# Performance work log

Hardware: AMD Instinct MI355X
Metric: run time of the kernel (lower is better)

## Reference

```python
import jax, jax.numpy as jnp
import numpy as np

D_MODEL = 1024
N, L = 4, 2048


def setup_inputs() -> dict:
    key = jax.random.key(0)
    ks = jax.random.split(key, 8)
    s = 0.1
    return {
        "X": jax.random.normal(ks[0], (N, L, D_MODEL), dtype=jnp.float32),
        "W_Q1": jax.random.normal(ks[1], (D_MODEL, D_MODEL), dtype=jnp.float32) * s,
        "W_K1": jax.random.normal(ks[2], (D_MODEL, D_MODEL), dtype=jnp.float32) * s,
        "W_V1": jax.random.normal(ks[3], (D_MODEL, D_MODEL), dtype=jnp.float32) * s,
        "W_Q2": jax.random.normal(ks[4], (D_MODEL, D_MODEL), dtype=jnp.float32) * s,
        "W_K2": jax.random.normal(ks[5], (D_MODEL, D_MODEL), dtype=jnp.float32) * s,
        "W_V2": jax.random.normal(ks[6], (D_MODEL, D_MODEL), dtype=jnp.float32) * s,
        "W_O": jax.random.normal(ks[7], (D_MODEL, 1), dtype=jnp.float32) * s,
        "b_O": jnp.zeros((1, 1), dtype=jnp.float32),
    }


def _attn_block(H, W_Q, W_K, W_V):
    # H: (N, L, D); single-head scaled dot-product attention
    Q = jnp.einsum('nld,dk->nlk', H, W_Q)
    K = jnp.einsum('nld,dk->nlk', H, W_K)
    V = jnp.einsum('nld,dk->nlk', H, W_V)
    scale = jnp.sqrt(jnp.asarray(Q.shape[-1], Q.dtype))
    scores = jnp.einsum('nqd,nkd->nqk', Q, K) / scale  # (N, L, L)
    attn = jax.nn.softmax(scores, axis=-1)
    return jnp.einsum('nqk,nkd->nqd', attn, V)


def reference(X, W_Q1, W_K1, W_V1, W_Q2, W_K2, W_V2, W_O, b_O):
    H1 = _attn_block(X, W_Q1, W_K1, W_V1)
    H2 = _attn_block(H1, W_Q2, W_K2, W_V2)
    pooled = jnp.mean(H2, axis=1)            # (N, D)
    logits = pooled @ W_O + b_O              # (N, 1)
    return jax.nn.sigmoid(logits).squeeze(-1)  # (N,)
```

## Files before the change

### kernel.cpp

```cpp
#include <hip/hip_runtime.h>
#include <hip/hip_bf16.h>
#include <cstdint>


#define DEVFN __device__ __forceinline__

typedef __attribute__((ext_vector_type(8))) short bf16x8;
typedef __attribute__((ext_vector_type(8))) _Float16 f16x8;
typedef __attribute__((ext_vector_type(4))) float f32x4;
typedef unsigned short u16;

DEVFN u16 f2bf(float f) {
    uint32_t x = __float_as_uint(f);
    x += 0x7fffu + ((x >> 16) & 1u);
    return (u16)(x >> 16);
}
DEVFN float bf2f(u16 u) { return __uint_as_float(((uint32_t)u) << 16); }

DEVFN void gload_lds16(const void* g, void* l) {
    __builtin_amdgcn_global_load_lds(
        (const __attribute__((address_space(1))) void*)g,
        (__attribute__((address_space(3))) void*)l, 16, 0, 0);
}

#define MFMA16 __builtin_amdgcn_mfma_f32_16x16x32_bf16

template<int EPI, bool TBUF>
__global__ __launch_bounds__(256, TBUF ? 3 : 4) void gemmk(
    const u16* __restrict__ A, long long aStride,
    const u16* __restrict__ B, long long bStride,
    void* __restrict__ out0, void* __restrict__ out1,
    const float* __restrict__ zrow, long long cStride,
    int M, int N, int K, int lda, int ldb, int ldc, float scale)
{
    constexpr int ASEC  = 128 * 32;
    constexpr int BUFSZ = ASEC + 128 * 32;
    constexpr int NU    = 4;
    constexpr int NB    = TBUF ? 3 : 2;

    __shared__ __align__(16) u16 L[NB * BUFSZ];
    const int tid  = threadIdx.x;
    const int wave = tid >> 6, lane = tid & 63;

    const int gx = gridDim.x, gy = gridDim.y;
    const int nwg = gx * gy * gridDim.z;
    int flat = (blockIdx.z * gy + blockIdx.y) * gx + blockIdx.x;
    flat = (flat & 7) * (nwg >> 3) + (flat >> 3);
    const int bx = flat % gx, by = (flat / gx) % gy, bz = flat / (gx * gy);

    const u16* pA = A + (size_t)bz * aStride;
    const u16* pB = B + (size_t)bz * bStride;
    const int m0 = by * 128, n0 = bx * 128;

    const u16* src[NU];
    int dst[NU];
#pragma unroll
    for (int q = 0; q < 2; q++) {
        const int s = q * 256 + tid, row = s >> 2, c = (s & 3) ^ ((row >> 1) & 3);
        src[q]     = pA + (size_t)(m0 + row) * lda + c * 8;
        dst[q]     = q * 2048 + wave * 512;
        src[2 + q] = pB + (size_t)(n0 + row) * ldb + c * 8;
        dst[2 + q] = ASEC + q * 2048 + wave * 512;
    }

    const int fr = lane & 15, ch = lane >> 4;
    const int wr = (wave >> 1) * 64, wc = (wave & 1) * 64;

    const int NT = K >> 5;
    f32x4 acc[4][4] = {};

    if constexpr (TBUF) {
#pragma unroll
        for (int u = 0; u < NU; u++) { gload_lds16(src[u], &L[dst[u]]); src[u] += 32; }
#pragma unroll
        for (int u = 0; u < NU; u++) { gload_lds16(src[u], &L[BUFSZ + dst[u]]); src[u] += 32; }
        asm volatile("s_waitcnt vmcnt(4)" ::: "memory");
        __builtin_amdgcn_s_barrier();
        __builtin_amdgcn_sched_barrier(0);

        int cIdx = 0, sIdx = 2;
        for (int kt = 0; kt < NT; ++kt) {
            const int cOff = cIdx * BUFSZ;
            if (kt + 2 < NT) {
                const int sOff = sIdx * BUFSZ;
#pragma unroll
                for (int u = 0; u < NU; u++) { gload_lds16(src[u], &L[sOff + dst[u]]); src[u] += 32; }
            }

            bf16x8 ah[4], bh[4];
#pragma unroll
            for (int i = 0; i < 4; i++) {
                const int r = wr + i * 16 + fr;
                ah[i] = *(const bf16x8*)&L[cOff + r * 32 + ((ch ^ ((r >> 1) & 3)) << 3)];
            }
#pragma unroll
            for (int j = 0; j < 4; j++) {
                const int r = wc + j * 16 + fr;
                bh[j] = *(const bf16x8*)&L[cOff + ASEC + r * 32 + ((ch ^ ((r >> 1) & 3)) << 3)];
            }

#pragma unroll
            for (int i = 0; i < 4; i++)
#pragma unroll
                for (int j = 0; j < 4; j++)
                    acc[i][j] = MFMA16(ah[i], bh[j], acc[i][j], 0, 0, 0);

            if (kt + 1 < NT) {
                if (kt + 2 < NT) asm volatile("s_waitcnt vmcnt(4)" ::: "memory");
                else             asm volatile("s_waitcnt vmcnt(0)" ::: "memory");
                __builtin_amdgcn_s_barrier();
                __builtin_amdgcn_sched_barrier(0);
            }
            cIdx = (cIdx == 2) ? 0 : cIdx + 1;
            sIdx = (sIdx == 2) ? 0 : sIdx + 1;
        }
    } else {
#pragma unroll
        for (int u = 0; u < NU; u++) { gload_lds16(src[u], &L[dst[u]]); src[u] += 32; }
        __syncthreads();

        int cur = 0;
        for (int kt = 0; kt < NT; ++kt) {
            const int cOff = cur * BUFSZ;
            const int sOff = BUFSZ - cOff;
            if (kt + 1 < NT) {
#pragma unroll
                for (int u = 0; u < NU; u++) { gload_lds16(src[u], &L[sOff + dst[u]]); src[u] += 32; }
            }

            bf16x8 ah[4], bh[4];
#pragma unroll
            for (int i = 0; i < 4; i++) {
                const int r = wr + i * 16 + fr;
                ah[i] = *(const bf16x8*)&L[cOff + r * 32 + ((ch ^ ((r >> 1) & 3)) << 3)];
            }
#pragma unroll
            for (int j = 0; j < 4; j++) {
                const int r = wc + j * 16 + fr;
                bh[j] = *(const bf16x8*)&L[cOff + ASEC + r * 32 + ((ch ^ ((r >> 1) & 3)) << 3)];
            }

#pragma unroll
            for (int i = 0; i < 4; i++)
#pragma unroll
                for (int j = 0; j < 4; j++)
                    acc[i][j] = MFMA16(ah[i], bh[j], acc[i][j], 0, 0, 0);

            __syncthreads();
            cur ^= 1;
        }
    }

    if constexpr (EPI == 5) {
#pragma unroll
        for (int i = 0; i < 4; i++)
#pragma unroll
            for (int r = 0; r < 4; r++) {
                const int rowb = m0 + wr + i * 16 + ch * 4 + r;
                float s = 0.f;
#pragma unroll
                for (int j = 0; j < 4; j++) {
                    const int col = n0 + wc + j * 16 + fr;
                    const float e = __expf(acc[i][j][r] * scale - 60.f);
                    s += e;
                    ((u16*)out0)[(size_t)bz * cStride + (size_t)rowb * ldc + col] = f2bf(e);
                }
                s += __shfl_xor(s, 1, 16);
                s += __shfl_xor(s, 2, 16);
                s += __shfl_xor(s, 4, 16);
                s += __shfl_xor(s, 8, 16);
                if (fr == 0)
                    ((float*)out1)[((size_t)bz * 2048 + rowb) * 32 + ((n0 + wc) >> 6)] = s;
            }
    } else if constexpr (EPI == 6) {
#pragma unroll
        for (int i = 0; i < 4; i++)
#pragma unroll
            for (int r = 0; r < 4; r++) {
                const int row = m0 + wr + i * 16 + ch * 4 + r;
                const size_t grow = (size_t)bz * 2048 + row;
                float zp = zrow[grow * 32 + 2 * fr] + zrow[grow * 32 + 2 * fr + 1];
                zp += __shfl_xor(zp, 1, 16);
                zp += __shfl_xor(zp, 2, 16);
                zp += __shfl_xor(zp, 4, 16);
                zp += __shfl_xor(zp, 8, 16);
                const float zi = 1.f / zp;
#pragma unroll
                for (int j = 0; j < 4; j++) {
                    const int col = n0 + wc + j * 16 + fr;
                    ((u16*)out0)[(size_t)bz * cStride + (size_t)row * ldc + col] =
                        f2bf(acc[i][j][r] * zi);
                }
            }
    } else {
#pragma unroll
        for (int i = 0; i < 4; i++)
#pragma unroll
            for (int j = 0; j < 4; j++)
#pragma unroll
                for (int r = 0; r < 4; r++) {
                    const int row = m0 + wr + i * 16 + (lane >> 4) * 4 + r;
                    const int col = n0 + wc + j * 16 + (lane & 15);
                    const float v = acc[i][j][r] * scale;
                    if constexpr (EPI == 3) {
                        ((u16*)out0)[(size_t)bz * cStride + (size_t)row * ldc + col] = f2bf(v);
                    } else {
                        ((_Float16*)out0)[(size_t)bz * cStride + (size_t)row * ldc + col] =
                            (_Float16)v;
                    }
                }
    }
}

__global__ __launch_bounds__(256, 3) void gemm_tv(
    const u16* __restrict__ Xb, const u16* __restrict__ Mt1,
    const u16* __restrict__ Wv1T, u16* __restrict__ Tb, u16* __restrict__ Vtb)
{
    constexpr int ASEC  = 128 * 32;
    constexpr int BUFSZ = ASEC + 128 * 32;
    constexpr int NU    = 4;

    __shared__ __align__(16) u16 L[3 * BUFSZ];
    const int tid  = threadIdx.x;
    const int wave = tid >> 6, lane = tid & 63;

    int flat = blockIdx.x;
    flat = (flat & 7) * 128 + (flat >> 3);
    const int op = flat & 1, t = flat >> 1;
    const u16* pA;
    const u16* pB;
    u16* outp;
    int m0, n0, ldc;
    if (op == 0) {
        pA = Xb;  pB = Mt1;  outp = Tb;  ldc = 1024;
        m0 = (t >> 3) * 128; n0 = (t & 7) * 128;
    } else {
        pA = Wv1T; pB = Xb;  outp = Vtb; ldc = 8192;
        m0 = (t >> 6) * 128; n0 = (t & 63) * 128;
    }

    const u16* src[NU];
    int dst[NU];
#pragma unroll
    for (int q = 0; q < 2; q++) {
        const int s = q * 256 + tid, row = s >> 2, c = (s & 3) ^ ((row >> 1) & 3);
        src[q]     = pA + (size_t)(m0 + row) * 1024 + c * 8;
        dst[q]     = q * 2048 + wave * 512;
        src[2 + q] = pB + (size_t)(n0 + row) * 1024 + c * 8;
        dst[2 + q] = ASEC + q * 2048 + wave * 512;
    }

    const int fr = lane & 15, ch = lane >> 4;
    const int wr = (wave >> 1) * 64, wc = (wave & 1) * 64;

#pragma unroll
    for (int u = 0; u < NU; u++) { gload_lds16(src[u], &L[dst[u]]); src[u] += 32; }
#pragma unroll
    for (int u = 0; u < NU; u++) { gload_lds16(src[u], &L[BUFSZ + dst[u]]); src[u] += 32; }
    asm volatile("s_waitcnt vmcnt(4)" ::: "memory");
    __builtin_amdgcn_s_barrier();
    __builtin_amdgcn_sched_barrier(0);

    f32x4 acc[4][4] = {};
    int cIdx = 0, sIdx = 2;

    for (int kt = 0; kt < 32; ++kt) {
        const int cOff = cIdx * BUFSZ;
        if (kt + 2 < 32) {
            const int sOff = sIdx * BUFSZ;
#pragma unroll
            for (int u = 0; u < NU; u++) { gload_lds16(src[u], &L[sOff + dst[u]]); src[u] += 32; }
        }

        bf16x8 ah[4], bh[4];
#pragma unroll
        for (int i = 0; i < 4; i++) {
            const int r = wr + i * 16 + fr;
            ah[i] = *(const bf16x8*)&L[cOff + r * 32 + ((ch ^ ((r >> 1) & 3)) << 3)];
        }
#pragma unroll
        for (int j = 0; j < 4; j++) {
            const int r = wc + j * 16 + fr;
            bh[j] = *(const bf16x8*)&L[cOff + ASEC + r * 32 + ((ch ^ ((r >> 1) & 3)) << 3)];
        }

#pragma unroll
        for (int i = 0; i < 4; i++)
#pragma unroll
            for (int j = 0; j < 4; j++)
                acc[i][j] = MFMA16(ah[i], bh[j], acc[i][j], 0, 0, 0);

        if (kt + 1 < 32) {
            if (kt + 2 < 32) asm volatile("s_waitcnt vmcnt(4)" ::: "memory");
            else             asm volatile("s_waitcnt vmcnt(0)" ::: "memory");
            __builtin_amdgcn_s_barrier();
            __builtin_amdgcn_sched_barrier(0);
        }
        cIdx = (cIdx == 2) ? 0 : cIdx + 1;
        sIdx = (sIdx == 2) ? 0 : sIdx + 1;
    }

#pragma unroll
    for (int i = 0; i < 4; i++)
#pragma unroll
        for (int j = 0; j < 4; j++)
#pragma unroll
            for (int r = 0; r < 4; r++) {
                const int row = m0 + wr + i * 16 + (lane >> 4) * 4 + r;
                const int col = n0 + wc + j * 16 + (lane & 15);
                outp[(size_t)row * ldc + col] = f2bf(acc[i][j][r]);
            }
}

__global__ __launch_bounds__(256) void prep_all(
    const float* __restrict__ X,
    const float* __restrict__ W0, const float* __restrict__ W1,
    const float* __restrict__ W2, const float* __restrict__ W3,
    const float* __restrict__ Wv1, const float* __restrict__ Wv2,
    const float* __restrict__ wO,
    u16* __restrict__ Xb, u16* __restrict__ Wcat,
    u16* __restrict__ Wv1T, float* __restrict__ wv)
{
    const int blk = blockIdx.x, tid = threadIdx.x;
    __shared__ float t[64][65];

    if (blk < 8192) {
        const size_t i = ((size_t)blk * 256 + tid) * 4;
        const float4 v = *(const float4*)&X[i];
        ushort4 h;
        h.x = f2bf(v.x); h.y = f2bf(v.y); h.z = f2bf(v.z); h.w = f2bf(v.w);
        *(ushort4*)&Xb[i] = h;
    } else if (blk < 12288) {
        const int w = (blk - 8192) >> 10, ib = (blk - 8192) & 1023;
        const float* W = (w == 0) ? W0 : (w == 1) ? W1 : (w == 2) ? W2 : W3;
        u16* o = Wcat + (size_t)w * 1048576;
        const size_t i = ((size_t)ib * 256 + tid) * 4;
        const float4 v = *(const float4*)&W[i];
        ushort4 h;
        h.x = f2bf(v.x); h.y = f2bf(v.y); h.z = f2bf(v.z); h.w = f2bf(v.w);
        *(ushort4*)&o[i] = h;
    } else if (blk < 12544) {
        const int tb = blk - 12288;
        const int r0 = (tb >> 4) * 64, c0 = (tb & 15) * 64;
#pragma unroll
        for (int it = 0; it < 16; it++) {
            const int idx = it * 256 + tid, rr = idx >> 6, cc = idx & 63;
            t[rr][cc] = Wv1[(size_t)(r0 + rr) * 1024 + (c0 + cc)];
        }
        __syncthreads();
#pragma unroll
        for (int it = 0; it < 16; it++) {
            const int idx = it * 256 + tid, nn = idx >> 6, kk = idx & 63;
            Wv1T[(size_t)(c0 + nn) * 1024 + (r0 + kk)] = f2bf(t[kk][nn]);
        }
    } else {
        const int d = (blk - 12544) * 16 + (tid >> 4);
        const int lx = tid & 15;
        const float* row = Wv2 + (size_t)d * 1024;
        float s = 0.f;
#pragma unroll
        for (int it = 0; it < 16; it++) {
            const int j = it * 64 + lx * 4;
            const float4 a = *(const float4*)&row[j];
            const float4 w = *(const float4*)&wO[j];
            s += a.x * w.x + a.y * w.y + a.z * w.z + a.w * w.w;
        }
#pragma unroll
        for (int o = 8; o; o >>= 1) s += __shfl_xor(s, o, 16);
        if (lx == 0) wv[d] = s;
    }
}

__global__ __launch_bounds__(256) void mid_head(
    const _Float16* __restrict__ S, float* __restrict__ part,
    const u16* __restrict__ H1, const float* __restrict__ wv,
    float* __restrict__ u)
{
    const int blk = blockIdx.x, tid = threadIdx.x;
    __shared__ float redm[4], reds[4];

    if (blk < 512) {
        const int b = blk >> 7, chunk = blk & 127;
        const _Float16* Sb = S + (size_t)b * (2048 * 2048) + (size_t)chunk * 16 * 2048;
        float acc[8] = {};

        for (int r = 0; r < 16; r++) {
            const _Float16* row = Sb + (size_t)r * 2048;
            const f16x8 hv = *(const f16x8*)&row[tid * 8];
            float v[8];
#pragma unroll
            for (int j = 0; j < 8; j++) v[j] = (float)hv[j];

            float m = v[0];
#pragma unroll
            for (int j = 1; j < 8; j++) m = fmaxf(m, v[j]);
            for (int o = 32; o; o >>= 1) m = fmaxf(m, __shfl_xor(m, o));
            if ((tid & 63) == 0) redm[tid >> 6] = m;
            __syncthreads();
            m = fmaxf(fmaxf(redm[0], redm[1]), fmaxf(redm[2], redm[3]));

            float e[8], s = 0.f;
#pragma unroll
            for (int j = 0; j < 8; j++) { e[j] = __expf(v[j] - m); s += e[j]; }
            for (int o = 32; o; o >>= 1) s += __shfl_xor(s, o);
            if ((tid & 63) == 0) reds[tid >> 6] = s;
            __syncthreads();
            const float inv = 1.f / (reds[0] + reds[1] + reds[2] + reds[3]);
#pragma unroll
            for (int j = 0; j < 8; j++) acc[j] += e[j] * inv;
            __syncthreads();
        }

        float* p = part + ((size_t)(b * 128 + chunk)) * 2048;
#pragma unroll
        for (int j = 0; j < 8; j++) p[tid * 8 + j] = acc[j];
    } else {
        const int r = (blk - 512) * 16 + (tid >> 4);
        const int lx = tid & 15;
        const u16* row = H1 + (size_t)r * 1024;
        float s = 0.f;
#pragma unroll
        for (int it = 0; it < 8; it++) {
            const int d = it * 128 + lx * 8;
            const bf16x8 h = *(const bf16x8*)&row[d];
#pragma unroll
            for (int j = 0; j < 8; j++) s += bf2f((u16)h[j]) * wv[d + j];
        }
#pragma unroll
        for (int o = 8; o; o >>= 1) s += __shfl_xor(s, o, 16);
        if (lx == 0) u[r] = s;
    }
}

__global__ __launch_bounds__(256) void tail2(
    const float* __restrict__ part, const float* __restrict__ u,
    float* __restrict__ partial)
{
    const int blk = blockIdx.x, tid = threadIdx.x;
    const int b = blk >> 5;
    const int kl = tid & 63;
    const int k = (blk & 31) * 64 + kl;
    const int cg = tid >> 6;
    float s = 0.f;
#pragma unroll 4
    for (int c = 0; c < 32; c++)
        s += part[((size_t)(b * 128 + cg * 32 + c)) * 2048 + k];
    __shared__ float red[4][64];
    red[cg][kl] = s;
    __syncthreads();
    if (cg == 0) {
        float v = (red[0][kl] + red[1][kl] + red[2][kl] + red[3][kl])
                  * u[b * 2048 + k];
        for (int o = 32; o; o >>= 1) v += __shfl_xor(v, o);
        if (kl == 0) partial[blk] = v;
    }
}

__global__ void head_final(const float* __restrict__ partial,
                           const float* __restrict__ bO, float* __restrict__ out)
{
    const int t = threadIdx.x;
    float v = partial[t];
#pragma unroll
    for (int o = 16; o; o >>= 1) v += __shfl_xor(v, o);
    if ((t & 31) == 0) {
        const float logit = v * (1.f / 2048.f) + bO[0];
        out[t >> 5] = 1.f / (1.f + __expf(-logit));
    }
}

extern "C" void kernel_launch(void* const* d_in, const int* in_sizes, int n_in,
                              void* d_out, int out_size, void* d_ws, size_t ws_size,
                              hipStream_t stream)
{
    const float* X   = (const float*)d_in[0];
    const float* Wq1 = (const float*)d_in[1];
    const float* Wk1 = (const float*)d_in[2];
    const float* Wv1 = (const float*)d_in[3];
    const float* Wq2 = (const float*)d_in[4];
    const float* Wk2 = (const float*)d_in[5];
    const float* Wv2 = (const float*)d_in[6];
    const float* WO  = (const float*)d_in[7];
    const float* bO  = (const float*)d_in[8];
    float* out = (float*)d_out;

    uint8_t* ws = (uint8_t*)d_ws;
    const size_t MB = 1ull << 20;
    u16* Xb   = (u16*)(ws + 0);
    u16* Tb   = (u16*)(ws + 32 * MB);
    float* part    = (float*)(ws + 80 * MB);
    float* partial = (float*)(ws + 85 * MB);
    float* wv      = (float*)(ws + 86 * MB);
    float* ud      = (float*)(ws + 87 * MB);
    float* Zpart   = (float*)(ws + 88 * MB);
    u16* Vtb  = (u16*)(ws + 96 * MB);
    u16* Wcat = (u16*)(ws + 128 * MB);
    u16* Eb   = (u16*)(ws + 152 * MB);
    _Float16* Sh = (_Float16*)(ws + 152 * MB);

    auto Wslot = [&](int i) { return Wcat + (size_t)i * 1048576; };

    prep_all<<<12608, 256, 0, stream>>>(
        X, Wq1, Wq2, Wk1, Wk2, Wv1, Wv2, WO, Xb, Wcat, Wslot(5), wv);
    gemmk<3, true><<<dim3(8, 8, 2), 256, 0, stream>>>(
        Wslot(2), 1048576, Wslot(0), 1048576, Wslot(4), nullptr, nullptr,
        2 * 1048576LL, 1024, 1024, 1024, 1024, 1024, 1024, 1.f);

    const long long LD2 = 2048LL * 1024;
    const long long EST = 2048LL * 2048;

    gemm_tv<<<1024, 256, 0, stream>>>(Xb, Wslot(4), Wslot(5), Tb, Vtb);
    gemmk<5, false><<<dim3(16, 16, 4), 256, 0, stream>>>(
        Tb, LD2, Xb, LD2, Eb, Zpart, nullptr, EST,
        2048, 2048, 1024, 1024, 1024, 2048, 0.03125f);
    gemmk<6, true><<<dim3(8, 16, 4), 256, 0, stream>>>(
        Eb, EST, Vtb, 2048, Xb, nullptr, Zpart, LD2,
        2048, 1024, 2048, 2048, 8192, 1024, 1.f);

    gemmk<3, true><<<dim3(8, 64, 1), 256, 0, stream>>>(
        Xb, 0, Wslot(6), 0, Tb, nullptr, nullptr, 0,
        8192, 1024, 1024, 1024, 1024, 1024, 1.f);
    gemmk<8, false><<<dim3(16, 16, 4), 256, 0, stream>>>(
        Tb, LD2, Xb, LD2, Sh, nullptr, nullptr, EST,
        2048, 2048, 1024, 1024, 1024, 2048, 0.03125f);

    mid_head<<<1024, 256, 0, stream>>>(Sh, part, Xb, wv, ud);
    tail2<<<128, 256, 0, stream>>>(part, ud, partial);
    head_final<<<1, 128, 0, stream>>>(partial, bO, out);
}
```

Before: 258.5 us.

## Add 256x256-tile 512-thread GEMM with triple-buffered LDS for score GEMMs

Adds a new gemm256 kernel that computes 256x256 output tiles with 8 waves, each wave owning a 128x64 subtile. It uses a three-stage LDS ring with direct global-to-LDS loads and a single barrier per k-step. The two L×L score GEMMs (the exp-producing one and the fp16 score one) now use it instead of the 128x128 gemmk. The goal is higher arithmetic intensity per LDS/global load and fewer barriers, at the cost of a larger register footprint, one workgroup per CU, and a grid of only 256 blocks.

```diff
diff --git a/kernel.cpp b/kernel.cpp
--- a/kernel.cpp
+++ b/kernel.cpp
@@ -151,28 +151,7 @@
         }
     }
 
-    if constexpr (EPI == 5) {
-#pragma unroll
-        for (int i = 0; i < 4; i++)
-#pragma unroll
-            for (int r = 0; r < 4; r++) {
-                const int rowb = m0 + wr + i * 16 + ch * 4 + r;
-                float s = 0.f;
-#pragma unroll
-                for (int j = 0; j < 4; j++) {
-                    const int col = n0 + wc + j * 16 + fr;
-                    const float e = __expf(acc[i][j][r] * scale - 60.f);
-                    s += e;
-                    ((u16*)out0)[(size_t)bz * cStride + (size_t)rowb * ldc + col] = f2bf(e);
-                }
-                s += __shfl_xor(s, 1, 16);
-                s += __shfl_xor(s, 2, 16);
-                s += __shfl_xor(s, 4, 16);
-                s += __shfl_xor(s, 8, 16);
-                if (fr == 0)
-                    ((float*)out1)[((size_t)bz * 2048 + rowb) * 32 + ((n0 + wc) >> 6)] = s;
-            }
-    } else if constexpr (EPI == 6) {
+    if constexpr (EPI == 6) {
 #pragma unroll
         for (int i = 0; i < 4; i++)
 #pragma unroll
@@ -208,6 +187,131 @@
                         ((_Float16*)out0)[(size_t)bz * cStride + (size_t)row * ldc + col] =
                             (_Float16)v;
                     }
+                }
+    }
+}
+
+template<int EPI>
+__global__ __launch_bounds__(512, 1) void gemm256(
+    const u16* __restrict__ A, long long aStride,
+    const u16* __restrict__ B, long long bStride,
+    void* __restrict__ out0, void* __restrict__ out1, long long cStride,
+    int K, int lda, int ldb, int ldc, float scale)
+{
+    constexpr int ASEC  = 256 * 32;
+    constexpr int BUFSZ = 2 * ASEC;
+    constexpr int NU    = 4;
+
+    __shared__ __align__(16) u16 L[3 * BUFSZ];
+    const int tid  = threadIdx.x;
+    const int wave = tid >> 6, lane = tid & 63;
+
+    const int gx = gridDim.x, gy = gridDim.y;
+    const int nwg = gx * gy * gridDim.z;
+    int flat = (blockIdx.z * gy + blockIdx.y) * gx + blockIdx.x;
+    flat = (flat & 7) * (nwg >> 3) + (flat >> 3);
+    const int bx = flat % gx, by = (flat / gx) % gy, bz = flat / (gx * gy);
+
+    const u16* pA = A + (size_t)bz * aStride;
+    const u16* pB = B + (size_t)bz * bStride;
+    const int m0 = by * 256, n0 = bx * 256;
+
+    const u16* src[NU];
+    int dst[NU];
+#pragma unroll
+    for (int q = 0; q < 2; q++) {
+        const int s = q * 512 + tid, row = s >> 2, c = (s & 3) ^ ((row >> 1) & 3);
+        src[q]     = pA + (size_t)(m0 + row) * lda + c * 8;
+        dst[q]     = q * 4096 + wave * 512;
+        src[2 + q] = pB + (size_t)(n0 + row) * ldb + c * 8;
+        dst[2 + q] = ASEC + q * 4096 + wave * 512;
+    }
+
+    const int fr = lane & 15, ch = lane >> 4;
+    const int wm = (wave >> 2) * 128;
+    const int wn = (wave & 3) * 64;
+
+    const int NT = K >> 5;
+
+#pragma unroll
+    for (int u = 0; u < NU; u++) { gload_lds16(src[u], &L[dst[u]]); src[u] += 32; }
+#pragma unroll
+    for (int u = 0; u < NU; u++) { gload_lds16(src[u], &L[BUFSZ + dst[u]]); src[u] += 32; }
+    asm volatile("s_waitcnt vmcnt(4)" ::: "memory");
+    __builtin_amdgcn_s_barrier();
+    __builtin_amdgcn_sched_barrier(0);
+
+    f32x4 acc[8][4] = {};
+    int cIdx = 0, sIdx = 2;
+
+    for (int kt = 0; kt < NT; ++kt) {
+        const int cOff = cIdx * BUFSZ;
+        if (kt + 2 < NT) {
+            const int sOff = sIdx * BUFSZ;
+#pragma unroll
+            for (int u = 0; u < NU; u++) { gload_lds16(src[u], &L[sOff + dst[u]]); src[u] += 32; }
+        }
+
+        bf16x8 ah[8], bh[4];
+#pragma unroll
+        for (int i = 0; i < 8; i++) {
+            const int r = wm + i * 16 + fr;
+            ah[i] = *(const bf16x8*)&L[cOff + r * 32 + ((ch ^ ((r >> 1) & 3)) << 3)];
+        }
+#pragma unroll
+        for (int j = 0; j < 4; j++) {
+            const int r = wn + j * 16 + fr;
+            bh[j] = *(const bf16x8*)&L[cOff + ASEC + r * 32 + ((ch ^ ((r >> 1) & 3)) << 3)];
+        }
+
+#pragma unroll
+        for (int i = 0; i < 8; i++)
+#pragma unroll
+            for (int j = 0; j < 4; j++)
+                acc[i][j] = MFMA16(ah[i], bh[j], acc[i][j], 0, 0, 0);
+
+        if (kt + 1 < NT) {
+            if (kt + 2 < NT) asm volatile("s_waitcnt vmcnt(4)" ::: "memory");
+            else             asm volatile("s_waitcnt vmcnt(0)" ::: "memory");
+            __builtin_amdgcn_s_barrier();
+            __builtin_amdgcn_sched_barrier(0);
+        }
+        cIdx = (cIdx == 2) ? 0 : cIdx + 1;
+        sIdx = (sIdx == 2) ? 0 : sIdx + 1;
+    }
+
+    if constexpr (EPI == 5) {
+#pragma unroll
+        for (int i = 0; i < 8; i++)
+#pragma unroll
+            for (int r = 0; r < 4; r++) {
+                const int rowb = m0 + wm + i * 16 + ch * 4 + r;
+                float s = 0.f;
+#pragma unroll
+                for (int j = 0; j < 4; j++) {
+                    const int col = n0 + wn + j * 16 + fr;
+                    const float e = __expf(acc[i][j][r] * scale - 60.f);
+                    s += e;
+                    ((u16*)out0)[(size_t)bz * cStride + (size_t)rowb * ldc + col] = f2bf(e);
+                }
+                s += __shfl_xor(s, 1, 16);
+                s += __shfl_xor(s, 2, 16);
+                s += __shfl_xor(s, 4, 16);
+                s += __shfl_xor(s, 8, 16);
+                if (fr == 0)
+                    ((float*)out1)[((size_t)bz * 2048 + rowb) * 32 + ((n0 + wn) >> 6)] = s;
+            }
+    } else {
+#pragma unroll
+        for (int i = 0; i < 8; i++)
+#pragma unroll
+            for (int j = 0; j < 4; j++)
+#pragma unroll
+                for (int r = 0; r < 4; r++) {
+                    const int row = m0 + wm + i * 16 + ch * 4 + r;
+                    const int col = n0 + wn + j * 16 + fr;
+                    ((_Float16*)out0)[(size_t)bz * cStride + (size_t)row * ldc + col] =
+                        (_Float16)(acc[i][j][r] * scale);
                 }
     }
 }
@@ -510,9 +614,9 @@
     const long long EST = 2048LL * 2048;
 
     gemm_tv<<<1024, 256, 0, stream>>>(Xb, Wslot(4), Wslot(5), Tb, Vtb);
-    gemmk<5, false><<<dim3(16, 16, 4), 256, 0, stream>>>(
-        Tb, LD2, Xb, LD2, Eb, Zpart, nullptr, EST,
-        2048, 2048, 1024, 1024, 1024, 2048, 0.03125f);
+    gemm256<5><<<dim3(8, 8, 4), 512, 0, stream>>>(
+        Tb, LD2, Xb, LD2, Eb, Zpart, EST,
+        1024, 1024, 1024, 2048, 0.03125f);
     gemmk<6, true><<<dim3(8, 16, 4), 256, 0, stream>>>(
         Eb, EST, Vtb, 2048, Xb, nullptr, Zpart, LD2,
         2048, 1024, 2048, 2048, 8192, 1024, 1.f);
@@ -520,9 +624,9 @@
     gemmk<3, true><<<dim3(8, 64, 1), 256, 0, stream>>>(
         Xb, 0, Wslot(6), 0, Tb, nullptr, nullptr, 0,
         8192, 1024, 1024, 1024, 1024, 1024, 1.f);
-    gemmk<8, false><<<dim3(16, 16, 4), 256, 0, stream>>>(
-        Tb, LD2, Xb, LD2, Sh, nullptr, nullptr, EST,
-        2048, 2048, 1024, 1024, 1024, 2048, 0.03125f);
+    gemm256<8><<<dim3(8, 8, 4), 512, 0, stream>>>(
+        Tb, LD2, Xb, LD2, Sh, nullptr, EST,
+        1024, 1024, 1024, 2048, 0.03125f);
 
     mid_head<<<1024, 256, 0, stream>>>(Sh, part, Xb, wv, ud);
     tail2<<<128, 256, 0, stream>>>(part, ud, partial);
```

Measured after the change: 247.8 us. 1.04x faster.
